# Performance work log

Hardware: AMD Instinct MI355X
Metric: run time of the kernel (lower is better)

## Reference

```python
import jax, jax.numpy as jnp
import numpy as np

B, T, C = 4, 2048, 1024
H, D = 16, 64
EPS = 1.1920929e-07  # torch.finfo(float32).eps, used by F.rms_norm default


def setup_inputs() -> dict:
    key = jax.random.key(0)
    ks = jax.random.split(key, 6)
    x = jax.random.normal(ks[0], (B, T, C), dtype=jnp.float32)
    # rotary cache: theta = 10000^(-2i/D), broadcastable [1, T, 1, D//2]
    inv_freq = 1.0 / (10000.0 ** (jnp.arange(0, D // 2, dtype=jnp.float32) * 2.0 / D))
    ang = jnp.arange(T, dtype=jnp.float32)[:, None] * inv_freq[None, :]  # [T, D//2]
    cos = jnp.cos(ang)[None, :, None, :]
    sin = jnp.sin(ang)[None, :, None, :]
    s = 0.02
    Wq = jax.random.normal(ks[1], (C, C), dtype=jnp.float32) * s
    Wk = jax.random.normal(ks[2], (C, C), dtype=jnp.float32) * s
    Wv = jax.random.normal(ks[3], (C, C), dtype=jnp.float32) * s
    Wo = jax.random.normal(ks[4], (C, C), dtype=jnp.float32) * s
    return {"x": x, "cos": cos, "sin": sin, "Wq": Wq, "Wk": Wk, "Wv": Wv, "Wo": Wo}


def _rope(x, cos, sin):
    d = x.shape[-1] // 2
    x1, x2 = x[..., :d], x[..., d:]
    return jnp.concatenate([x1 * cos + x2 * sin, -x1 * sin + x2 * cos], axis=-1)


def _rmsnorm(x):
    ms = jnp.mean(jnp.square(x), axis=-1, keepdims=True)
    return x * jax.lax.rsqrt(ms + EPS)


def reference(x, cos, sin, Wq, Wk, Wv, Wo):
    Bx, Tx, Cx = x.shape
    q = (x @ Wq.T).reshape(Bx, Tx, H, D)
    k = (x @ Wk.T).reshape(Bx, Tx, H, D)
    v = (x @ Wv.T).reshape(Bx, Tx, H, D)
    q = _rmsnorm(_rope(q, cos, sin))
    k = _rmsnorm(_rope(k, cos, sin))
    scale = 1.0 / jnp.sqrt(jnp.float32(D))
    # non-causal SDPA
    scores = jnp.einsum('bthd,bshd->bhts', q, k) * scale  # [B,H,T,T]
    attn = jax.nn.softmax(scores, axis=-1)
    y = jnp.einsum('bhts,bshd->bthd', attn, v).reshape(Bx, Tx, Cx)
    return y @ Wo.T
```

## Files before the change

### kernel.cpp

```cpp
#include <hip/hip_runtime.h>

#define B_ 4
#define T_ 2048
#define C_ 1024
#define H_ 16
#define D_ 64
#define EPS_ 1.1920929e-07f
#define LOG2E_ 1.4426950408889634f

typedef __attribute__((ext_vector_type(8))) short bf16x8;
typedef __attribute__((ext_vector_type(4))) float f32x4;
typedef __attribute__((ext_vector_type(16))) float f32x16;
typedef unsigned short u16;
typedef unsigned int u32;
typedef __attribute__((ext_vector_type(4))) u32 u32x4;

__device__ inline u16 f2bf(float f) {
  unsigned u = __float_as_uint(f);
  unsigned r = (u + 0x7fffu + ((u >> 16) & 1u)) >> 16;
  return (u16)r;
}

__device__ __forceinline__ void gload16(const void* g, void* l) {
  __builtin_amdgcn_global_load_lds(
      (__attribute__((address_space(1))) void*)g,
      (__attribute__((address_space(3))) void*)l, 16, 0, 0);
}

__global__ __launch_bounds__(256) void cvt_bf16(const float* __restrict__ src,
                                                u16* __restrict__ dst, int n) {
  const int i = (blockIdx.x * 256 + threadIdx.x) * 4;
  if (i < n) {
    float4 v = *(const float4*)&src[i];
    ushort4 o;
    o.x = f2bf(v.x); o.y = f2bf(v.y); o.z = f2bf(v.z); o.w = f2bf(v.w);
    *(ushort4*)&dst[i] = o;
  }
}

__global__ __launch_bounds__(256) void cvt_weights(const float* __restrict__ wq,
                                                   const float* __restrict__ wk,
                                                   const float* __restrict__ wv,
                                                   const float* __restrict__ wo,
                                                   u16* __restrict__ wqkv,
                                                   u16* __restrict__ wob, int n) {
  const int i = (blockIdx.x * 256 + threadIdx.x) * 4;
  const int t = blockIdx.y;
  const float* src = (t == 0) ? wq : (t == 1) ? wk : (t == 2) ? wv : wo;
  u16* dst = (t == 3) ? wob : (wqkv + (size_t)t * n);
  if (i < n) {
    float4 v = *(const float4*)&src[i];
    ushort4 o;
    o.x = f2bf(v.x); o.y = f2bf(v.y); o.z = f2bf(v.z); o.w = f2bf(v.w);
    *(ushort4*)&dst[i] = o;
  }
}

__global__ __launch_bounds__(256) void gemm_qkv(const u16* __restrict__ X,
                                                const u16* __restrict__ W,
                                                u16* __restrict__ qb,
                                                u16* __restrict__ kb,
                                                u16* __restrict__ vtb,
                                                const float* __restrict__ cs,
                                                const float* __restrict__ sn,
                                                int M, int K) {
  __shared__ short As[128 * 64];
  __shared__ short Bs[128 * 64];
  const int tid = threadIdx.x;
  const int lane = tid & 63;
  const int w = tid >> 6;
  const int wr = w >> 1, wc = w & 1;
  const int m0 = blockIdx.y * 128, n0 = blockIdx.x * 128;
  const int lrow = lane >> 3;
  const int lcol = (lane & 7) * 8;

  f32x4 acc[4][4];
#pragma unroll
  for (int mi = 0; mi < 4; ++mi)
#pragma unroll
    for (int ni = 0; ni < 4; ++ni)
      acc[mi][ni] = (f32x4){0.f, 0.f, 0.f, 0.f};

  const int r = lane & 15;
  const int quad = lane >> 4;

  for (int kt = 0; kt < K; kt += 64) {
#pragma unroll
    for (int i = 0; i < 4; ++i) {
      const int row = w * 32 + i * 8;
      gload16(&X[(size_t)(m0 + row + lrow) * K + kt + lcol], &As[row * 64]);
      gload16(&W[(size_t)(n0 + row + lrow) * K + kt + lcol], &Bs[row * 64]);
    }
    __syncthreads();
#pragma unroll
    for (int kc = 0; kc < 2; ++kc) {
      const int ko = kc * 32 + quad * 8;
      bf16x8 a[4], b[4];
#pragma unroll
      for (int mi = 0; mi < 4; ++mi)
        a[mi] = *(const bf16x8*)&As[(wr * 64 + mi * 16 + r) * 64 + ko];
#pragma unroll
      for (int ni = 0; ni < 4; ++ni)
        b[ni] = *(const bf16x8*)&Bs[(wc * 64 + ni * 16 + r) * 64 + ko];
#pragma unroll
      for (int mi = 0; mi < 4; ++mi)
#pragma unroll
        for (int ni = 0; ni < 4; ++ni)
          acc[mi][ni] = __builtin_amdgcn_mfma_f32_16x16x32_bf16(a[mi], b[ni], acc[mi][ni], 0, 0, 0);
    }
    __syncthreads();
  }

  const int which = blockIdx.x >> 3;
  const int c0 = (blockIdx.x & 7) * 128 + wc * 64;

  if (which < 2) {
    u16* dst = (which == 0) ? qb : kb;
#pragma unroll
    for (int mi = 0; mi < 4; ++mi)
#pragma unroll
      for (int j = 0; j < 4; ++j) {
        const int gr = m0 + wr * 64 + mi * 16 + quad * 4 + j;
        const int t = gr & (T_ - 1);
        float o[4];
#pragma unroll
        for (int ni = 0; ni < 2; ++ni) {
          const float c = cs[t * 32 + ni * 16 + r];
          const float s = sn[t * 32 + ni * 16 + r];
          const float x1 = acc[mi][ni][j], x2 = acc[mi][ni + 2][j];
          o[ni]     = x1 * c + x2 * s;
          o[ni + 2] = x2 * c - x1 * s;
        }
        float sq = o[0] * o[0] + o[1] * o[1] + o[2] * o[2] + o[3] * o[3];
        sq += __shfl_xor(sq, 1, 64);
        sq += __shfl_xor(sq, 2, 64);
        sq += __shfl_xor(sq, 4, 64);
        sq += __shfl_xor(sq, 8, 64);
        float rn = rsqrtf(sq * (1.0f / 64.0f) + EPS_);
        if (which == 0) rn *= 0.125f * LOG2E_;
#pragma unroll
        for (int ni = 0; ni < 4; ++ni)
          dst[(size_t)gr * C_ + c0 + ni * 16 + r] = f2bf(o[ni] * rn);
      }
  } else {
    const int h = (blockIdx.x & 7) * 2 + wc;
    const int gr0 = m0 + wr * 64;
    const int bb = gr0 >> 11;
    const int tbase = gr0 & (T_ - 1);
#pragma unroll
    for (int ni = 0; ni < 4; ++ni) {
      const int d = ni * 16 + r;
      u16* rowp = &vtb[((size_t)((bb * H_ + h) * D_ + d)) * T_ + tbase];
#pragma unroll
      for (int mi = 0; mi < 4; ++mi) {
        u32 lo, hi2;
        asm("v_cvt_pk_bf16_f32 %0, %1, %2" : "=v"(lo) : "v"(acc[mi][ni][0]), "v"(acc[mi][ni][1]));
        asm("v_cvt_pk_bf16_f32 %0, %1, %2" : "=v"(hi2) : "v"(acc[mi][ni][2]), "v"(acc[mi][ni][3]));
        u16* p = rowp + mi * 16 + quad * 2;
        *(u32*)&p[0] = lo;
        *(u32*)&p[8] = hi2;
      }
    }
  }
}

__global__ __launch_bounds__(256) void gemm_out(const u16* __restrict__ X,
                                                const u16* __restrict__ W,
                                                float* __restrict__ Y,
                                                int M, int N, int K) {
  __shared__ short As[128 * 64];
  __shared__ short Bs[128 * 64];
  const int tid = threadIdx.x;
  const int lane = tid & 63;
  const int w = tid >> 6;
  const int wr = w >> 1, wc = w & 1;
  const int m0 = blockIdx.y * 128, n0 = blockIdx.x * 128;
  const int lrow = lane >> 3;
  const int lcol = (lane & 7) * 8;

  f32x4 acc[4][4];
#pragma unroll
  for (int mi = 0; mi < 4; ++mi)
#pragma unroll
    for (int ni = 0; ni < 4; ++ni)
      acc[mi][ni] = (f32x4){0.f, 0.f, 0.f, 0.f};

  const int r = lane & 15;
  const int quad = lane >> 4;

  for (int kt = 0; kt < K; kt += 64) {
#pragma unroll
    for (int i = 0; i < 4; ++i) {
      const int row = w * 32 + i * 8;
      gload16(&X[(size_t)(m0 + row + lrow) * K + kt + lcol], &As[row * 64]);
      gload16(&W[(size_t)(n0 + row + lrow) * K + kt + lcol], &Bs[row * 64]);
    }
    __syncthreads();
#pragma unroll
    for (int kc = 0; kc < 2; ++kc) {
      const int ko = kc * 32 + quad * 8;
      bf16x8 a[4], b[4];
#pragma unroll
      for (int mi = 0; mi < 4; ++mi)
        a[mi] = *(const bf16x8*)&As[(wr * 64 + mi * 16 + r) * 64 + ko];
#pragma unroll
      for (int ni = 0; ni < 4; ++ni)
        b[ni] = *(const bf16x8*)&Bs[(wc * 64 + ni * 16 + r) * 64 + ko];
#pragma unroll
      for (int mi = 0; mi < 4; ++mi)
#pragma unroll
        for (int ni = 0; ni < 4; ++ni)
          acc[mi][ni] = __builtin_amdgcn_mfma_f32_16x16x32_bf16(a[mi], b[ni], acc[mi][ni], 0, 0, 0);
    }
    __syncthreads();
  }

#pragma unroll
  for (int mi = 0; mi < 4; ++mi)
#pragma unroll
    for (int ni = 0; ni < 4; ++ni) {
      const int gc = n0 + wc * 64 + ni * 16 + r;
#pragma unroll
      for (int j = 0; j < 4; ++j) {
        const int gr = m0 + wr * 64 + mi * 16 + quad * 4 + j;
        Y[(size_t)gr * N + gc] = acc[mi][ni][j];
      }
    }
}

__global__ __launch_bounds__(256) void flash_mfma(const u16* __restrict__ Qb,
                                                  const u16* __restrict__ Kb,
                                                  const u16* __restrict__ Vtb,
                                                  u16* __restrict__ Yb) {
  __shared__ u16 Ks[2][64][72];
  __shared__ u16 Vt[2][64][72];
  const int tid = threadIdx.x;
  const int lane = tid & 63;
  const int w = tid >> 6;
  const int c = lane & 31;
  const int hi = lane >> 5;
  const int bh = blockIdx.x, qt = blockIdx.y;
  const int b = bh >> 4, h = bh & 15;
  const int srow = lane;
  const int sd0 = w * 16;
  const int vrow = tid >> 2;
  const int vco = (tid & 3) * 16;

  bf16x8 k0, k1, v0, v1;
  {
    const size_t gk = ((size_t)((b * T_ + srow) * H_ + h)) * D_ + sd0;
    k0 = *(const bf16x8*)&Kb[gk];
    k1 = *(const bf16x8*)&Kb[gk + 8];
    const size_t gv = ((size_t)(bh * 64 + vrow)) * T_ + vco;
    v0 = *(const bf16x8*)&Vtb[gv];
    v1 = *(const bf16x8*)&Vtb[gv + 8];
  }

  {
    const int row = tid >> 1, half = tid & 1;
    const size_t g = ((size_t)((b * T_ + qt * 128 + row) * H_ + h)) * D_ + half * 32;
    u16* qd = (row < 64) ? &Ks[0][row][half * 32] : &Ks[1][row - 64][half * 32];
    *(bf16x8*)&qd[0]  = *(const bf16x8*)&Qb[g];
    *(bf16x8*)&qd[8]  = *(const bf16x8*)&Qb[g + 8];
    *(bf16x8*)&qd[16] = *(const bf16x8*)&Qb[g + 16];
    *(bf16x8*)&qd[24] = *(const bf16x8*)&Qb[g + 24];
  }
  __syncthreads();
  bf16x8 qf[4];
  {
    const int qr = w * 32 + c;
    const u16* qs = (qr < 64) ? &Ks[0][qr][0] : &Ks[1][qr - 64][0];
#pragma unroll
    for (int ks = 0; ks < 4; ++ks)
      qf[ks] = *(const bf16x8*)&qs[ks * 16 + hi * 8];
  }
  __syncthreads();

  *(bf16x8*)&Ks[0][srow][sd0] = k0;
  *(bf16x8*)&Ks[0][srow][sd0 + 8] = k1;
  *(bf16x8*)&Vt[0][vrow][vco] = v0;
  *(bf16x8*)&Vt[0][vrow][vco + 8] = v1;
  {
    const size_t gk = ((size_t)((b * T_ + 64 + srow) * H_ + h)) * D_ + sd0;
    k0 = *(const bf16x8*)&Kb[gk];
    k1 = *(const bf16x8*)&Kb[gk + 8];
    const size_t gv = ((size_t)(bh * 64 + vrow)) * T_ + 64 + vco;
    v0 = *(const bf16x8*)&Vtb[gv];
    v1 = *(const bf16x8*)&Vtb[gv + 8];
  }
  __syncthreads();

  f32x16 oacc[2];
  oacc[0] = (f32x16)(0.f);
  oacc[1] = (f32x16)(0.f);
  float l_acc = 0.f;

  const int NT = T_ / 64;
  for (int t = 0; t < NT; ++t) {
    const int cur = t & 1;

    f32x16 s0 = (f32x16)(0.f), s1 = (f32x16)(0.f);
#pragma unroll
    for (int ks = 0; ks < 4; ++ks) {
      bf16x8 kf0 = *(const bf16x8*)&Ks[cur][c][ks * 16 + hi * 8];
      bf16x8 kf1 = *(const bf16x8*)&Ks[cur][32 + c][ks * 16 + hi * 8];
      s0 = __builtin_amdgcn_mfma_f32_32x32x16_bf16(kf0, qf[ks], s0, 0, 0, 0);
      s1 = __builtin_amdgcn_mfma_f32_32x32x16_bf16(kf1, qf[ks], s1, 0, 0, 0);
    }

    if (t + 1 < NT) {
      const int nxt = cur ^ 1;
      *(bf16x8*)&Ks[nxt][srow][sd0] = k0;
      *(bf16x8*)&Ks[nxt][srow][sd0 + 8] = k1;
      *(bf16x8*)&Vt[nxt][vrow][vco] = v0;
      *(bf16x8*)&Vt[nxt][vrow][vco + 8] = v1;
      if (t + 2 < NT) {
        const size_t gk = ((size_t)((b * T_ + (t + 2) * 64 + srow) * H_ + h)) * D_ + sd0;
        k0 = *(const bf16x8*)&Kb[gk];
        k1 = *(const bf16x8*)&Kb[gk + 8];
        const size_t gv = ((size_t)(bh * 64 + vrow)) * T_ + (t + 2) * 64 + vco;
        v0 = *(const bf16x8*)&Vtb[gv];
        v1 = *(const bf16x8*)&Vtb[gv + 8];
      }
    }

    u32 wrd[2][4][2];
#pragma unroll
    for (int m = 0; m < 4; ++m)
#pragma unroll
      for (int p = 0; p < 2; ++p) {
        float a0 = __builtin_amdgcn_exp2f(s0[m * 4 + p * 2]);
        float a1 = __builtin_amdgcn_exp2f(s0[m * 4 + p * 2 + 1]);
        float b0 = __builtin_amdgcn_exp2f(s1[m * 4 + p * 2]);
        float b1 = __builtin_amdgcn_exp2f(s1[m * 4 + p * 2 + 1]);
        l_acc += (a0 + a1) + (b0 + b1);
        asm("v_cvt_pk_bf16_f32 %0, %1, %2" : "=v"(wrd[0][m][p]) : "v"(a0), "v"(a1));
        asm("v_cvt_pk_bf16_f32 %0, %1, %2" : "=v"(wrd[1][m][p]) : "v"(b0), "v"(b1));
      }
#pragma unroll
    for (int kt2 = 0; kt2 < 2; ++kt2)
#pragma unroll
      for (int m = 0; m < 4; ++m)
        asm("v_permlane32_swap_b32 %0, %1" : "+v"(wrd[kt2][m][0]), "+v"(wrd[kt2][m][1]));

    bf16x8 pa[4];
    pa[0] = __builtin_bit_cast(bf16x8, (u32x4){wrd[0][0][0], wrd[0][0][1], wrd[0][1][0], wrd[0][1][1]});
    pa[1] = __builtin_bit_cast(bf16x8, (u32x4){wrd[0][2][0], wrd[0][2][1], wrd[0][3][0], wrd[0][3][1]});
    pa[2] = __builtin_bit_cast(bf16x8, (u32x4){wrd[1][0][0], wrd[1][0][1], wrd[1][1][0], wrd[1][1][1]});
    pa[3] = __builtin_bit_cast(bf16x8, (u32x4){wrd[1][2][0], wrd[1][2][1], wrd[1][3][0], wrd[1][3][1]});

#pragma unroll
    for (int ks = 0; ks < 4; ++ks) {
      bf16x8 vf0 = *(const bf16x8*)&Vt[cur][c][ks * 16 + hi * 8];
      bf16x8 vf1 = *(const bf16x8*)&Vt[cur][32 + c][ks * 16 + hi * 8];
      oacc[0] = __builtin_amdgcn_mfma_f32_32x32x16_bf16(pa[ks], vf0, oacc[0], 0, 0, 0);
      oacc[1] = __builtin_amdgcn_mfma_f32_32x32x16_bf16(pa[ks], vf1, oacc[1], 0, 0, 0);
    }
    __syncthreads();
  }

  float l_all = l_acc + __shfl_xor(l_acc, 32, 64);
#pragma unroll
  for (int v = 0; v < 16; ++v) {
    const int q = (v & 3) + 8 * (v >> 2) + 4 * hi;
    const float inv = 1.0f / __shfl(l_all, q, 64);
    const int tq = qt * 128 + w * 32 + q;
    const size_t gbase = ((size_t)((b * T_ + tq) * H_ + h)) * D_;
    Yb[gbase + c]      = f2bf(oacc[0][v] * inv);
    Yb[gbase + 32 + c] = f2bf(oacc[1][v] * inv);
  }
}

extern "C" void kernel_launch(void* const* d_in, const int* in_sizes, int n_in,
                              void* d_out, int out_size, void* d_ws, size_t ws_size,
                              hipStream_t stream) {
  const float* x    = (const float*)d_in[0];
  const float* cosb = (const float*)d_in[1];
  const float* sinb = (const float*)d_in[2];
  const float* Wq   = (const float*)d_in[3];
  const float* Wk   = (const float*)d_in[4];
  const float* Wv   = (const float*)d_in[5];
  const float* Wo   = (const float*)d_in[6];
  float* out = (float*)d_out;

  const size_t NE = (size_t)B_ * T_ * C_;
  const int CC = C_ * C_;
  u16* xb   = (u16*)d_ws;
  u16* qb   = xb + NE;
  u16* kb   = qb + NE;
  u16* vtb  = kb + NE;
  u16* wqkv = vtb + NE;
  u16* wob  = wqkv + 3 * (size_t)CC;
  u16* yb   = xb;

  const int M = B_ * T_;

  cvt_bf16<<<(int)(NE / 1024), 256, 0, stream>>>(x, xb, (int)NE);
  dim3 wg(CC / 1024, 4);
  cvt_weights<<<wg, 256, 0, stream>>>(Wq, Wk, Wv, Wo, wqkv, wob, CC);

  dim3 qg(24, M / 128), gb(256);
  gemm_qkv<<<qg, gb, 0, stream>>>(xb, wqkv, qb, kb, vtb, cosb, sinb, M, C_);

  dim3 fg(B_ * H_, T_ / 128);
  flash_mfma<<<fg, 256, 0, stream>>>(qb, kb, vtb, yb);

  dim3 og(C_ / 128, M / 128);
  gemm_out<<<og, gb, 0, stream>>>(yb, wob, out, M, C_, C_);
}
```

Before: 312.9 us.

## Merge conversions, remap GEMM blocks, compute softmax denominator via MFMA

The two fp32-to-bf16 conversion kernels become one launch. Both GEMMs remap their block indices so that consecutive blocks are spread out, which changes L2 reuse and how work lands across XCDs. The flash kernel adds s_setprio around its MFMA sections, unrolls the loop by 2, and simplifies address math. It also drops the scalar row-sum plus shuffle and computes the softmax denominator with an extra MFMA against a ones vector. That extra MFMA adds matrix work and bf16 rounding to the denominator in exchange for fewer VALU adds and shuffles.

```diff
diff --git a/kernel.cpp b/kernel.cpp
--- a/kernel.cpp
+++ b/kernel.cpp
@@ -27,33 +27,34 @@
       (__attribute__((address_space(3))) void*)l, 16, 0, 0);
 }
 
-__global__ __launch_bounds__(256) void cvt_bf16(const float* __restrict__ src,
-                                                u16* __restrict__ dst, int n) {
-  const int i = (blockIdx.x * 256 + threadIdx.x) * 4;
-  if (i < n) {
-    float4 v = *(const float4*)&src[i];
-    ushort4 o;
-    o.x = f2bf(v.x); o.y = f2bf(v.y); o.z = f2bf(v.z); o.w = f2bf(v.w);
-    *(ushort4*)&dst[i] = o;
-  }
-}
-
-__global__ __launch_bounds__(256) void cvt_weights(const float* __restrict__ wq,
-                                                   const float* __restrict__ wk,
-                                                   const float* __restrict__ wv,
-                                                   const float* __restrict__ wo,
-                                                   u16* __restrict__ wqkv,
-                                                   u16* __restrict__ wob, int n) {
-  const int i = (blockIdx.x * 256 + threadIdx.x) * 4;
-  const int t = blockIdx.y;
-  const float* src = (t == 0) ? wq : (t == 1) ? wk : (t == 2) ? wv : wo;
-  u16* dst = (t == 3) ? wob : (wqkv + (size_t)t * n);
-  if (i < n) {
-    float4 v = *(const float4*)&src[i];
-    ushort4 o;
-    o.x = f2bf(v.x); o.y = f2bf(v.y); o.z = f2bf(v.z); o.w = f2bf(v.w);
-    *(ushort4*)&dst[i] = o;
-  }
+__global__ __launch_bounds__(256) void cvt_all(const float* __restrict__ x,
+                                               const float* __restrict__ wq,
+                                               const float* __restrict__ wk,
+                                               const float* __restrict__ wv,
+                                               const float* __restrict__ wo,
+                                               u16* __restrict__ xb,
+                                               u16* __restrict__ wqkv,
+                                               u16* __restrict__ wob) {
+  const int NXB = (int)((size_t)B_ * T_ * C_ / 1024);
+  const int WB = (C_ * C_) / 1024;
+  const int bid = blockIdx.x;
+  const float* src;
+  u16* dst;
+  int i;
+  if (bid < NXB) {
+    src = x; dst = xb; i = bid * 1024 + threadIdx.x * 4;
+  } else {
+    const int wb = bid - NXB;
+    const int t = wb / WB;
+    const int r = wb - t * WB;
+    src = (t == 0) ? wq : (t == 1) ? wk : (t == 2) ? wv : wo;
+    dst = (t == 3) ? wob : (wqkv + (size_t)t * (C_ * C_));
+    i = r * 1024 + threadIdx.x * 4;
+  }
+  float4 v = *(const float4*)&src[i];
+  ushort4 o;
+  o.x = f2bf(v.x); o.y = f2bf(v.y); o.z = f2bf(v.z); o.w = f2bf(v.w);
+  *(ushort4*)&dst[i] = o;
 }
 
 __global__ __launch_bounds__(256) void gemm_qkv(const u16* __restrict__ X,
@@ -70,7 +71,10 @@
   const int lane = tid & 63;
   const int w = tid >> 6;
   const int wr = w >> 1, wc = w & 1;
-  const int m0 = blockIdx.y * 128, n0 = blockIdx.x * 128;
+  const int hwlin = blockIdx.x + 24 * blockIdx.y;
+  const int lg = (hwlin & 7) * 192 + (hwlin >> 3);
+  const int bx = lg % 24, by = lg / 24;
+  const int m0 = by * 128, n0 = bx * 128;
   const int lrow = lane >> 3;
   const int lcol = (lane & 7) * 8;
 
@@ -111,8 +115,8 @@
     __syncthreads();
   }
 
-  const int which = blockIdx.x >> 3;
-  const int c0 = (blockIdx.x & 7) * 128 + wc * 64;
+  const int which = bx >> 3;
+  const int c0 = (bx & 7) * 128 + wc * 64;
 
   if (which < 2) {
     u16* dst = (which == 0) ? qb : kb;
@@ -143,7 +147,7 @@
           dst[(size_t)gr * C_ + c0 + ni * 16 + r] = f2bf(o[ni] * rn);
       }
   } else {
-    const int h = (blockIdx.x & 7) * 2 + wc;
+    const int h = (bx & 7) * 2 + wc;
     const int gr0 = m0 + wr * 64;
     const int bb = gr0 >> 11;
     const int tbase = gr0 & (T_ - 1);
@@ -174,7 +178,10 @@
   const int lane = tid & 63;
   const int w = tid >> 6;
   const int wr = w >> 1, wc = w & 1;
-  const int m0 = blockIdx.y * 128, n0 = blockIdx.x * 128;
+  const int hwlin = blockIdx.x + 8 * blockIdx.y;
+  const int lg = (hwlin & 7) * 64 + (hwlin >> 3);
+  const int bx = lg & 7, by = lg >> 3;
+  const int m0 = by * 128, n0 = bx * 128;
   const int lrow = lane >> 3;
   const int lcol = (lane & 7) * 8;
 
@@ -246,15 +253,15 @@
   const int vrow = tid >> 2;
   const int vco = (tid & 3) * 16;
 
+  const u16* kbase = Kb + ((size_t)(b * T_ + srow) * H_ + h) * D_ + sd0;
+  const u16* vbase = Vtb + ((size_t)(bh * 64 + vrow)) * T_ + vco;
+  const int KSTRIDE = 64 * H_ * D_;
+
   bf16x8 k0, k1, v0, v1;
-  {
-    const size_t gk = ((size_t)((b * T_ + srow) * H_ + h)) * D_ + sd0;
-    k0 = *(const bf16x8*)&Kb[gk];
-    k1 = *(const bf16x8*)&Kb[gk + 8];
-    const size_t gv = ((size_t)(bh * 64 + vrow)) * T_ + vco;
-    v0 = *(const bf16x8*)&Vtb[gv];
-    v1 = *(const bf16x8*)&Vtb[gv + 8];
-  }
+  k0 = *(const bf16x8*)&kbase[0];
+  k1 = *(const bf16x8*)&kbase[8];
+  v0 = *(const bf16x8*)&vbase[0];
+  v1 = *(const bf16x8*)&vbase[8];
 
   {
     const int row = tid >> 1, half = tid & 1;
@@ -280,26 +287,27 @@
   *(bf16x8*)&Ks[0][srow][sd0 + 8] = k1;
   *(bf16x8*)&Vt[0][vrow][vco] = v0;
   *(bf16x8*)&Vt[0][vrow][vco + 8] = v1;
-  {
-    const size_t gk = ((size_t)((b * T_ + 64 + srow) * H_ + h)) * D_ + sd0;
-    k0 = *(const bf16x8*)&Kb[gk];
-    k1 = *(const bf16x8*)&Kb[gk + 8];
-    const size_t gv = ((size_t)(bh * 64 + vrow)) * T_ + 64 + vco;
-    v0 = *(const bf16x8*)&Vtb[gv];
-    v1 = *(const bf16x8*)&Vtb[gv + 8];
-  }
+  k0 = *(const bf16x8*)&kbase[KSTRIDE];
+  k1 = *(const bf16x8*)&kbase[KSTRIDE + 8];
+  v0 = *(const bf16x8*)&vbase[64];
+  v1 = *(const bf16x8*)&vbase[64 + 8];
   __syncthreads();
 
-  f32x16 oacc[2];
+  f32x16 oacc[2], oacc_l;
   oacc[0] = (f32x16)(0.f);
   oacc[1] = (f32x16)(0.f);
-  float l_acc = 0.f;
+  oacc_l  = (f32x16)(0.f);
+  bf16x8 onesv;
+#pragma unroll
+  for (int i = 0; i < 8; ++i) onesv[i] = (short)0x3F80;
 
   const int NT = T_ / 64;
+#pragma unroll 2
   for (int t = 0; t < NT; ++t) {
     const int cur = t & 1;
 
     f32x16 s0 = (f32x16)(0.f), s1 = (f32x16)(0.f);
+    __builtin_amdgcn_s_setprio(1);
 #pragma unroll
     for (int ks = 0; ks < 4; ++ks) {
       bf16x8 kf0 = *(const bf16x8*)&Ks[cur][c][ks * 16 + hi * 8];
@@ -307,6 +315,7 @@
       s0 = __builtin_amdgcn_mfma_f32_32x32x16_bf16(kf0, qf[ks], s0, 0, 0, 0);
       s1 = __builtin_amdgcn_mfma_f32_32x32x16_bf16(kf1, qf[ks], s1, 0, 0, 0);
     }
+    __builtin_amdgcn_s_setprio(0);
 
     if (t + 1 < NT) {
       const int nxt = cur ^ 1;
@@ -315,12 +324,12 @@
       *(bf16x8*)&Vt[nxt][vrow][vco] = v0;
       *(bf16x8*)&Vt[nxt][vrow][vco + 8] = v1;
       if (t + 2 < NT) {
-        const size_t gk = ((size_t)((b * T_ + (t + 2) * 64 + srow) * H_ + h)) * D_ + sd0;
-        k0 = *(const bf16x8*)&Kb[gk];
-        k1 = *(const bf16x8*)&Kb[gk + 8];
-        const size_t gv = ((size_t)(bh * 64 + vrow)) * T_ + (t + 2) * 64 + vco;
-        v0 = *(const bf16x8*)&Vtb[gv];
-        v1 = *(const bf16x8*)&Vtb[gv + 8];
+        const int gk = (t + 2) * KSTRIDE;
+        k0 = *(const bf16x8*)&kbase[gk];
+        k1 = *(const bf16x8*)&kbase[gk + 8];
+        const int gv = (t + 2) * 64;
+        v0 = *(const bf16x8*)&vbase[gv];
+        v1 = *(const bf16x8*)&vbase[gv + 8];
       }
     }
 
@@ -333,7 +342,6 @@
         float a1 = __builtin_amdgcn_exp2f(s0[m * 4 + p * 2 + 1]);
         float b0 = __builtin_amdgcn_exp2f(s1[m * 4 + p * 2]);
         float b1 = __builtin_amdgcn_exp2f(s1[m * 4 + p * 2 + 1]);
-        l_acc += (a0 + a1) + (b0 + b1);
         asm("v_cvt_pk_bf16_f32 %0, %1, %2" : "=v"(wrd[0][m][p]) : "v"(a0), "v"(a1));
         asm("v_cvt_pk_bf16_f32 %0, %1, %2" : "=v"(wrd[1][m][p]) : "v"(b0), "v"(b1));
       }
@@ -349,21 +357,23 @@
     pa[2] = __builtin_bit_cast(bf16x8, (u32x4){wrd[1][0][0], wrd[1][0][1], wrd[1][1][0], wrd[1][1][1]});
     pa[3] = __builtin_bit_cast(bf16x8, (u32x4){wrd[1][2][0], wrd[1][2][1], wrd[1][3][0], wrd[1][3][1]});
 
+    __builtin_amdgcn_s_setprio(1);
 #pragma unroll
     for (int ks = 0; ks < 4; ++ks) {
       bf16x8 vf0 = *(const bf16x8*)&Vt[cur][c][ks * 16 + hi * 8];
       bf16x8 vf1 = *(const bf16x8*)&Vt[cur][32 + c][ks * 16 + hi * 8];
       oacc[0] = __builtin_amdgcn_mfma_f32_32x32x16_bf16(pa[ks], vf0, oacc[0], 0, 0, 0);
       oacc[1] = __builtin_amdgcn_mfma_f32_32x32x16_bf16(pa[ks], vf1, oacc[1], 0, 0, 0);
-    }
+      oacc_l  = __builtin_amdgcn_mfma_f32_32x32x16_bf16(pa[ks], onesv, oacc_l, 0, 0, 0);
+    }
+    __builtin_amdgcn_s_setprio(0);
     __syncthreads();
   }
 
-  float l_all = l_acc + __shfl_xor(l_acc, 32, 64);
 #pragma unroll
   for (int v = 0; v < 16; ++v) {
+    const float inv = 1.0f / oacc_l[v];
     const int q = (v & 3) + 8 * (v >> 2) + 4 * hi;
-    const float inv = 1.0f / __shfl(l_all, q, 64);
     const int tq = qt * 128 + w * 32 + q;
     const size_t gbase = ((size_t)((b * T_ + tq) * H_ + h)) * D_;
     Yb[gbase + c]      = f2bf(oacc[0][v] * inv);
@@ -395,9 +405,9 @@
 
   const int M = B_ * T_;
 
-  cvt_bf16<<<(int)(NE / 1024), 256, 0, stream>>>(x, xb, (int)NE);
-  dim3 wg(CC / 1024, 4);
-  cvt_weights<<<wg, 256, 0, stream>>>(Wq, Wk, Wv, Wo, wqkv, wob, CC);
+  const int NXB = (int)(NE / 1024);
+  const int NWB = 4 * (CC / 1024);
+  cvt_all<<<NXB + NWB, 256, 0, stream>>>(x, Wq, Wk, Wv, Wo, xb, wqkv, wob);
 
   dim3 qg(24, M / 128), gb(256);
   gemm_qkv<<<qg, gb, 0, stream>>>(xb, wqkv, qb, kb, vtb, cosb, sinb, M, C_);
```

Result: no change. 311.1 us (-0.6%).
